# Performance work log

Hardware: AMD Instinct MI355X
Metric: run time of the kernel (lower is better)

## Reference

```python
import jax, jax.numpy as jnp
import numpy as np

HALF = 32           # (input_channels - 1) // 2
HIDDEN = 160
OUT = 32
GRU_IN = 32         # use_intensity=False -> (input_channels - 1) // 2
B, T, C = 1024, 512, 65


def setup_inputs() -> dict:
    key = jax.random.key(0)
    ks = jax.random.split(key, 10)
    times = jnp.sort(jax.random.uniform(ks[0], (T,), dtype=jnp.float32)) * 10.0
    X = jax.random.uniform(ks[1], (B, T, C), dtype=jnp.float32)
    final_index = jax.random.randint(ks[2], (B,), 0, T)
    s_ih = 1.0 / np.sqrt(HIDDEN)
    w_ih = jax.random.uniform(ks[3], (3 * HIDDEN, GRU_IN), jnp.float32, -s_ih, s_ih)
    w_hh = jax.random.uniform(ks[4], (3 * HIDDEN, HIDDEN), jnp.float32, -s_ih, s_ih)
    b_ih = jax.random.uniform(ks[5], (3 * HIDDEN,), jnp.float32, -s_ih, s_ih)
    b_hh = jax.random.uniform(ks[6], (3 * HIDDEN,), jnp.float32, -s_ih, s_ih)
    s_l = 1.0 / np.sqrt(HIDDEN)
    lin_w = jax.random.uniform(ks[7], (OUT, HIDDEN), jnp.float32, -s_l, s_l)
    lin_b = jax.random.uniform(ks[8], (OUT,), jnp.float32, -s_l, s_l)
    return {"times": times, "X": X, "final_index": final_index,
            "w_ih": w_ih, "w_hh": w_hh, "b_ih": b_ih, "b_hh": b_hh,
            "lin_w": lin_w, "lin_b": lin_b}


def _gru_cell(x, h, w_ih, w_hh, b_ih, b_hh):
    gi = x @ w_ih.T + b_ih                     # [B, 3H]
    gh = h @ w_hh.T + b_hh                     # [B, 3H]
    ir, iz, inn = jnp.split(gi, 3, axis=-1)
    hr, hz, hn = jnp.split(gh, 3, axis=-1)
    r = jax.nn.sigmoid(ir + hr)
    z = jax.nn.sigmoid(iz + hz)
    n = jnp.tanh(inn + r * hn)
    return (1.0 - z) * n + z * h


def _step(Xi, h, dt, w_ih, w_hh, b_ih, b_hh):
    # Xi: [B, C] differenced increments; channel 0 = dt increment,
    # channels 1:1+HALF = observation flags, 1+HALF: = values.
    observation = jnp.max(Xi[:, 1:1 + HALF], axis=1) > 0.5      # [B]
    Xi_piece = Xi[:, 1 + HALF:]                                  # use_intensity=False
    Xi_piece = Xi_piece.at[:, 0].add(dt)
    new_h = _gru_cell(Xi_piece, h, w_ih, w_hh, b_ih, b_hh)
    h_upd = jnp.where(observation[:, None], new_h, h)
    dt_upd = dt + jnp.where(observation, 0.0, Xi[:, 0])
    # torch skips the whole update when no sample observed this step
    any_obs = jnp.any(observation)
    h = jnp.where(any_obs, h_upd, h)
    dt = jnp.where(any_obs, dt_upd, dt)
    return h, dt


def reference(times, X, final_index, w_ih, w_hh, b_ih, b_hh, lin_w, lin_b):
    # Differencing, as in the torch forward
    Xd = X.at[:, 1:, 1:1 + HALF].add(-X[:, :-1, 1:1 + HALF])
    Xd = Xd.at[:, 0, 0].add(-times[0])
    Xd = Xd.at[:, 1:, 0].add(-times[:-1])

    z0 = jnp.zeros((B, HIDDEN), dtype=X.dtype)
    dt0 = jnp.zeros((B,), dtype=X.dtype)
    h0, dt0 = _step(Xd[:, 0], z0, dt0, w_ih, w_hh, b_ih, b_hh)

    def body(carry, Xi):
        h, dt = carry
        # evolve(h, time_diff) is identity (GRU_dt variant)
        h, dt = _step(Xi, h, dt, w_ih, w_hh, b_ih, b_hh)
        return (h, dt), h

    xs = jnp.moveaxis(Xd[:, 1:], 1, 0)                # [T-1, B, C]
    (_, _), hs = jax.lax.scan(body, (h0, dt0), xs)    # hs: [T-1, B, H]
    out = jnp.concatenate([h0[None], hs], axis=0)     # [T, B, H]
    out = jnp.moveaxis(out, 0, 1)                     # [B, T, H]
    final = jnp.take_along_axis(out, final_index[:, None, None], axis=1)[:, 0]
    return final @ lin_w.T + lin_b
```

## Files before the change

### kernel.cpp

```cpp
#include <hip/hip_runtime.h>
#include <math.h>

#define B_SZ 1024
#define T_SZ 512
#define C_CH 65
#define HID  160
#define OUTD 32
#define M_ELEM 4
#define NBLK 256
#define NTHR 640

#define LOG2E 1.4426950408889634f

#define OBS_OFF 0
#define ANY_OFF  524288
#define XD0_OFF  526336
#define S_OFF    2623488
#define WHH_OFF  6817792
#define WIH_OFF  6971392
#define XPK_OFF  7002112

typedef float f32x4_t __attribute__((ext_vector_type(4)));
typedef short bf16x8_t __attribute__((ext_vector_type(8)));
typedef unsigned u32x2_t __attribute__((ext_vector_type(2)));
typedef unsigned u32x4_t __attribute__((ext_vector_type(4)));
union frag_u { u32x4_t u; bf16x8_t h; };

__device__ __forceinline__ unsigned short f2bf(float x) {
  unsigned int u = __float_as_uint(x);
  unsigned int r = ((u >> 16) & 1u) + 0x7FFFu;
  return (unsigned short)((u + r) >> 16);
}
__device__ __forceinline__ unsigned cvt_pk_bf16(float lo, float hi) {
  unsigned r;
  asm("v_cvt_pk_bf16_f32 %0, %1, %2" : "=v"(r) : "v"(lo), "v"(hi));
  return r;
}
__device__ __forceinline__ float exp2_f(float x) {
  float r; asm("v_exp_f32 %0, %1" : "=v"(r) : "v"(x)); return r;
}
__device__ __forceinline__ float rcp_f(float x) {
  float r; asm("v_rcp_f32 %0, %1" : "=v"(r) : "v"(x)); return r;
}
__device__ __forceinline__ int tabf(int r) {
  return ((r & 1) << 1) | (((r >> 1) & 1) << 4);
}

__global__ void k_zero(unsigned* __restrict__ anyv) {
  int i = blockIdx.x * blockDim.x + threadIdx.x;
  if (i < T_SZ) anyv[i] = 0u;
}

__global__ __launch_bounds__(256) void k_prep(const float* __restrict__ X,
                                              const float* __restrict__ times,
                                              unsigned char* __restrict__ obs,
                                              unsigned* __restrict__ anyv,
                                              float* __restrict__ xd0,
                                              unsigned short* __restrict__ xpk) {
  const int b = blockIdx.x;
  const float* Xb = X + (size_t)b * T_SZ * C_CH;
  for (int t = threadIdx.x; t < T_SZ; t += 256) {
    const float* cur = Xb + t * C_CH;
    const float* prv = cur - C_CH;
    float m = -1e30f;
    if (t == 0) {
      #pragma unroll
      for (int c = 1; c <= 32; ++c) m = fmaxf(m, cur[c]);
    } else {
      #pragma unroll
      for (int c = 1; c <= 32; ++c) m = fmaxf(m, cur[c] - prv[c]);
    }
    unsigned char o = (m > 0.5f) ? (unsigned char)1 : (unsigned char)0;
    obs[(size_t)b * T_SZ + t] = o;
    if (o) atomicOr(&anyv[t], 1u);
    xd0[(size_t)b * T_SZ + t] = cur[0] - times[(t == 0) ? 0 : (t - 1)];
    unsigned short* dst = xpk + ((size_t)b * T_SZ + t) * 32;
    #pragma unroll
    for (int c = 0; c < 32; ++c) dst[c] = f2bf(cur[33 + c]);
  }
}

__global__ __launch_bounds__(64) void k_dt(const unsigned char* __restrict__ obs,
                                           const unsigned* __restrict__ anyv,
                                           const float* __restrict__ xd0,
                                           const int* __restrict__ fidx,
                                           float2* __restrict__ S) {
  const int b = blockIdx.x;
  const int lane = threadIdx.x;
  const int t0 = lane * 8;
  const unsigned long long o8 =
      *(const unsigned long long*)(obs + (size_t)b * T_SZ + t0);
  const float4* xd4 = (const float4*)(xd0 + (size_t)b * T_SZ + t0);
  const float4 xa = xd4[0], xb = xd4[1];
  const uint4* av4 = (const uint4*)(anyv + t0);
  const uint4 aa = av4[0], ab = av4[1];
  const int fi = fidx[b];
  const float xv[8] = {xa.x, xa.y, xa.z, xa.w, xb.x, xb.y, xb.z, xb.w};
  const unsigned av[8] = {aa.x, aa.y, aa.z, aa.w, ab.x, ab.y, ab.z, ab.w};
  float run = 0.f;
  float dtl[8], fl[8];
  #pragma unroll
  for (int j = 0; j < 8; ++j) {
    const int o = (int)((o8 >> (8 * j)) & 0xffULL);
    const int any = (int)av[j];
    dtl[j] = run;
    if (any && !o) run += xv[j];
    fl[j] = (any && o && (t0 + j) <= fi) ? 1.f : 0.f;
  }
  float inc = run;
  #pragma unroll
  for (int off = 1; off < 64; off <<= 1) {
    float u = __shfl_up(inc, off, 64);
    if (lane >= off) inc += u;
  }
  const float excl = inc - run;
  #pragma unroll
  for (int j = 0; j < 8; ++j)
    S[(size_t)(t0 + j) * B_SZ + b] = make_float2(excl + dtl[j], fl[j]);
}

__global__ __launch_bounds__(256) void k_pack(const float* __restrict__ w_ih,
                                              const float* __restrict__ w_hh,
                                              unsigned short* __restrict__ whh_f,
                                              unsigned short* __restrict__ wih_f) {
  int i = blockIdx.x * 256 + threadIdx.x;
  if (i < 9600) {
    int l = i & 63; int kt = (i >> 6) % 5; int g = (i / 320) % 3; int q = i / 960;
    const float scl = (g < 2) ? -LOG2E : -2.f * LOG2E;
    int row = g * 160 + q * 16 + (l & 15);
    const float* src = w_hh + (size_t)row * HID + kt * 32 + (l >> 4) * 8;
    unsigned short* dst = whh_f + (size_t)i * 8;
    #pragma unroll
    for (int j = 0; j < 8; ++j) dst[j] = f2bf(scl * src[j]);
  } else if (i < 11520) {
    int i2 = i - 9600;
    int l = i2 & 63; int g = (i2 >> 6) % 3; int q = i2 / 192;
    const float scl = (g < 2) ? -LOG2E : -2.f * LOG2E;
    int row = g * 160 + q * 16 + (l & 15);
    const float* src = w_ih + (size_t)row * 32 + (l >> 4) * 8;
    unsigned short* dst = wih_f + (size_t)i2 * 8;
    #pragma unroll
    for (int j = 0; j < 8; ++j) dst[j] = f2bf(scl * src[j]);
  }
}

#define MFMA16 __builtin_amdgcn_mfma_f32_16x16x32_bf16

__global__ __launch_bounds__(NTHR) void k_scan(
    const unsigned short* __restrict__ xpk, const int* __restrict__ fidx,
    const float* __restrict__ w_ih,
    const float* __restrict__ b_ih, const float* __restrict__ b_hh,
    const float* __restrict__ lin_w, const float* __restrict__ lin_b,
    const float2* __restrict__ Sf,
    const unsigned short* __restrict__ whh_f, const unsigned short* __restrict__ wih_f,
    float* __restrict__ out)
{
  const int b0 = blockIdx.x * M_ELEM;
  const int tid = threadIdx.x;
  const int wid = tid >> 6;
  const int lane = tid & 63;
  const int q = wid;

  __shared__ __align__(16) unsigned short hbuf[2][800];
  __shared__ __align__(16) float hm[M_ELEM][HID];

  { unsigned* hz = (unsigned*)hbuf;
    for (int i = tid; i < 800; i += NTHR) hz[i] = 0u; }

  int maxfi = 0;
  #pragma unroll
  for (int e = 0; e < M_ELEM; ++e) maxfi = max(maxfi, fidx[b0 + e]);

  const int r16 = lane & 15;
  const int g4 = lane >> 4;
  const int elA = ((r16 >> 2) + (r16 & 3)) & 3;
  const int me = g4;

  const int rb_u16 = (elA * 96 + tabf(elA)) * 2 + g4 * 8;
  const int col = q * 16 + r16;
  const int wA_u16 = (g4 * 96 + tabf(g4)) * 2 + col;

  bf16x8_t whh_v[3][5];
  bf16x8_t wih_v[3];
  #pragma unroll
  for (int g = 0; g < 3; ++g) {
    #pragma unroll
    for (int kt = 0; kt < 5; ++kt)
      whh_v[g][kt] = *(const bf16x8_t*)(whh_f + ((size_t)((q * 3 + g) * 5 + kt) * 64 + lane) * 8);
    wih_v[g] = *(const bf16x8_t*)(wih_f + ((size_t)(q * 3 + g) * 64 + lane) * 8);
  }
  const float b_r  = -LOG2E * (b_ih[col] + b_hh[col]);
  const float b_z  = -LOG2E * (b_ih[160 + col] + b_hh[160 + col]);
  const float b_ni = -2.f * LOG2E * b_ih[320 + col];
  const float b_nh = -2.f * LOG2E * b_hh[320 + col];
  const float w0r = -LOG2E * w_ih[(size_t)col * 32];
  const float w0z = -LOG2E * w_ih[(size_t)(160 + col) * 32];
  const float w0n = -2.f * LOG2E * w_ih[(size_t)(320 + col) * 32];

  float h = 0.f;
  const f32x4_t z4 = {0.f, 0.f, 0.f, 0.f};

  const unsigned short* xpk_base =
      xpk + ((size_t)(b0 + elA) * T_SZ) * 32 + g4 * 8;

  bf16x8_t xe = *(const bf16x8_t*)(xpk_base);
  bf16x8_t xo = *(const bf16x8_t*)(xpk_base + (size_t)min(1, maxfi) * 32);
  float2 se = Sf[b0 + me];
  float2 so = Sf[(size_t)min(1, maxfi) * B_SZ + b0 + me];
  __syncthreads();

  const int NSTEP = (maxfi + 2) & ~1;

#define BODY(T, PB, XI, SI)                                                \
  {                                                                        \
                         \
    frag_u hf0, hf1, hf2, hf3, hf4;                                        \
    {                                                                      \
      const u32x2_t* hp = (const u32x2_t*)&hbuf[PB][rb_u16];               \
      u32x2_t l0 = hp[0],  u0 = hp[1];                                     \
      u32x2_t l1 = hp[8],  u1 = hp[9];                                     \
      u32x2_t l2 = hp[16], u2 = hp[17];                                    \
      u32x2_t l3 = hp[24], u3 = hp[25];                                    \
      u32x2_t l4 = hp[32], u4 = hp[33];                                    \
      hf0.u = (u32x4_t){l0.x, l0.y, u0.x, u0.y};                           \
      hf1.u = (u32x4_t){l1.x, l1.y, u1.x, u1.y};                           \
      hf2.u = (u32x4_t){l2.x, l2.y, u2.x, u2.y};                           \
      hf3.u = (u32x4_t){l3.x, l3.y, u3.x, u3.y};                           \
      hf4.u = (u32x4_t){l4.x, l4.y, u4.x, u4.y};                           \
    }                                                                      \
          \
    f32x4_t ginr = MFMA16(XI, wih_v[0], z4, 0, 0, 0);                      \
    f32x4_t ginz = MFMA16(XI, wih_v[1], z4, 0, 0, 0);                      \
    f32x4_t ginn = MFMA16(XI, wih_v[2], z4, 0, 0, 0);                      \
               \
    const float crI = fmaf(SI.x, w0r, b_r);                                \
    const float czI = fmaf(SI.x, w0z, b_z);                                \
    const float cnI = fmaf(SI.x, w0n, b_ni);                               \
    const float flI = SI.y;                                                \
                    \
    __builtin_amdgcn_s_setprio(1);                                         \
    f32x4_t ra  = MFMA16(hf0.h, whh_v[0][0], ginr, 0, 0, 0);               \
    f32x4_t za  = MFMA16(hf0.h, whh_v[1][0], ginz, 0, 0, 0);               \
    f32x4_t nha = MFMA16(hf0.h, whh_v[2][0], z4,   0, 0, 0);               \
    f32x4_t rb  = MFMA16(hf2.h, whh_v[0][2], z4,   0, 0, 0);               \
    f32x4_t zb  = MFMA16(hf2.h, whh_v[1][2], z4,   0, 0, 0);               \
    f32x4_t nhb = MFMA16(hf3.h, whh_v[2][3], z4,   0, 0, 0);               \
    ra  = MFMA16(hf1.h, whh_v[0][1], ra,  0, 0, 0);                        \
    za  = MFMA16(hf1.h, whh_v[1][1], za,  0, 0, 0);                        \
    nha = MFMA16(hf1.h, whh_v[2][1], nha, 0, 0, 0);                        \
    rb  = MFMA16(hf3.h, whh_v[0][3], rb,  0, 0, 0);                        \
    zb  = MFMA16(hf3.h, whh_v[1][3], zb,  0, 0, 0);                        \
    nhb = MFMA16(hf4.h, whh_v[2][4], nhb, 0, 0, 0);                        \
    nha = MFMA16(hf2.h, whh_v[2][2], nha, 0, 0, 0);                        \
    rb  = MFMA16(hf4.h, whh_v[0][4], rb,  0, 0, 0);                        \
    zb  = MFMA16(hf4.h, whh_v[1][4], zb,  0, 0, 0);                        \
    __builtin_amdgcn_s_setprio(0);                                         \
              \
    {                                                                      \
      const int tl = min((T) + 2, T_SZ - 1);                               \
      XI = *(const bf16x8_t*)(xpk_base + (size_t)tl * 32);                 \
      SI = Sf[(size_t)tl * B_SZ + b0 + me];                                \
    }                                                                      \
                         \
    {                                                                      \
      const float pre_r = (ra[0] + rb[0]) + crI;                           \
      const float rr = rcp_f(1.f + exp2_f(pre_r));                         \
      const float pre_z = (za[0] + zb[0]) + czI;                           \
      const float zz = rcp_f(1.f + exp2_f(pre_z));                         \
      float u = (ginn[0] + cnI) + rr * ((nha[0] + nhb[0]) + b_nh);         \
      u = fminf(u, 60.f);                                                  \
      const float e = exp2_f(u);                                           \
      const float nn = (1.f - e) * rcp_f(1.f + e);                         \
      const float upd = nn + zz * (h - nn);                                \
      h = h + flI * (upd - h);                                             \
    }                                                                      \
                                             \
    hbuf[PB ^ 1][wA_u16] = (unsigned short)cvt_pk_bf16(h, h);              \
    __syncthreads();                                                       \
  }

  for (int t = 0; t < NSTEP; t += 2) {
    BODY(t,     0, xe, se);
    BODY(t + 1, 1, xo, so);
  }
#undef BODY

  hm[me][col] = h;
  __syncthreads();
  if (tid < M_ELEM * OUTD) {
    const int e = tid >> 5, o = tid & 31;
    const float4* lw = (const float4*)(lin_w + o * HID);
    const float4* hv = (const float4*)(&hm[e][0]);
    float a0 = 0.f, a1 = 0.f, a2 = 0.f, a3 = 0.f;
    #pragma unroll
    for (int k = 0; k < HID / 4; ++k) {
      float4 w = lw[k], hh = hv[k];
      a0 = fmaf(w.x, hh.x, a0); a1 = fmaf(w.y, hh.y, a1);
      a2 = fmaf(w.z, hh.z, a2); a3 = fmaf(w.w, hh.w, a3);
    }
    out[(size_t)(b0 + e) * OUTD + o] = lin_b[o] + (a0 + a1) + (a2 + a3);
  }
}

extern "C" void kernel_launch(void* const* d_in, const int* in_sizes, int n_in,
                              void* d_out, int out_size, void* d_ws, size_t ws_size,
                              hipStream_t stream) {
  const float* times = (const float*)d_in[0];
  const float* X     = (const float*)d_in[1];
  const int*   fidx  = (const int*)d_in[2];
  const float* w_ih  = (const float*)d_in[3];
  const float* w_hh  = (const float*)d_in[4];
  const float* b_ih  = (const float*)d_in[5];
  const float* b_hh  = (const float*)d_in[6];
  const float* lin_w = (const float*)d_in[7];
  const float* lin_b = (const float*)d_in[8];
  float* outp = (float*)d_out;

  unsigned char* obsb = (unsigned char*)d_ws + OBS_OFF;
  unsigned* anyv = (unsigned*)((char*)d_ws + ANY_OFF);
  float* xd0 = (float*)((char*)d_ws + XD0_OFF);
  float2* S = (float2*)((char*)d_ws + S_OFF);
  unsigned short* whh_f = (unsigned short*)((char*)d_ws + WHH_OFF);
  unsigned short* wih_f = (unsigned short*)((char*)d_ws + WIH_OFF);
  unsigned short* xpk = (unsigned short*)((char*)d_ws + XPK_OFF);

  k_zero<<<1, 512, 0, stream>>>(anyv);
  k_prep<<<B_SZ, 256, 0, stream>>>(X, times, obsb, anyv, xd0, xpk);
  k_dt<<<B_SZ, 64, 0, stream>>>(obsb, anyv, xd0, fidx, S);
  k_pack<<<45, 256, 0, stream>>>(w_ih, w_hh, whh_f, wih_f);
  k_scan<<<NBLK, NTHR, 0, stream>>>(xpk, fidx, w_ih, b_ih, b_hh,
                                    lin_w, lin_b, S, whh_f, wih_f, outp);
}
```

Measured before the change: 367.2 us.

## Stage per-step scalars in LDS and use single 16-byte hidden-state fragment loads

The per-step scalar array S is now stored batch-major and preloaded into shared memory for the block's four elements, so each step reads it from LDS instead of issuing a dependent global load. The hidden-state buffer padding (tabf) changes so each MFMA fragment can be read with one 16-byte LDS load instead of two 8-byte loads plus repacking. The gate update math is rewritten as fused multiply-adds, with tanh computed as 2*sigmoid-1. In exchange the block uses about 16KB more LDS, and the initial staging adds a short prologue.

```diff
diff --git a/kernel.cpp b/kernel.cpp
--- a/kernel.cpp
+++ b/kernel.cpp
@@ -22,9 +22,6 @@
 
 typedef float f32x4_t __attribute__((ext_vector_type(4)));
 typedef short bf16x8_t __attribute__((ext_vector_type(8)));
-typedef unsigned u32x2_t __attribute__((ext_vector_type(2)));
-typedef unsigned u32x4_t __attribute__((ext_vector_type(4)));
-union frag_u { u32x4_t u; bf16x8_t h; };
 
 __device__ __forceinline__ unsigned short f2bf(float x) {
   unsigned int u = __float_as_uint(x);
@@ -43,7 +40,7 @@
   float r; asm("v_rcp_f32 %0, %1" : "=v"(r) : "v"(x)); return r;
 }
 __device__ __forceinline__ int tabf(int r) {
-  return ((r & 1) << 1) | (((r >> 1) & 1) << 4);
+  return ((r & 1) << 2) | (((r >> 1) & 1) << 4);
 }
 
 __global__ void k_zero(unsigned* __restrict__ anyv) {
@@ -116,7 +113,7 @@
   const float excl = inc - run;
   #pragma unroll
   for (int j = 0; j < 8; ++j)
-    S[(size_t)(t0 + j) * B_SZ + b] = make_float2(excl + dtl[j], fl[j]);
+    S[(size_t)b * T_SZ + t0 + j] = make_float2(excl + dtl[j], fl[j]);
 }
 
 __global__ __launch_bounds__(256) void k_pack(const float* __restrict__ w_ih,
@@ -162,10 +159,15 @@
   const int q = wid;
 
   __shared__ __align__(16) unsigned short hbuf[2][800];
+  __shared__ __align__(8) float2 s_lds[T_SZ * M_ELEM];
   __shared__ __align__(16) float hm[M_ELEM][HID];
 
   { unsigned* hz = (unsigned*)hbuf;
     for (int i = tid; i < 800; i += NTHR) hz[i] = 0u; }
+  for (int i = tid; i < T_SZ * M_ELEM; i += NTHR) {
+    const int e = i >> 9, t = i & (T_SZ - 1);
+    s_lds[t * M_ELEM + e] = Sf[(size_t)(b0 + e) * T_SZ + t];
+  }
 
   int maxfi = 0;
   #pragma unroll
@@ -174,7 +176,6 @@
   const int r16 = lane & 15;
   const int g4 = lane >> 4;
   const int elA = ((r16 >> 2) + (r16 & 3)) & 3;
-  const int me = g4;
 
   const int rb_u16 = (elA * 96 + tabf(elA)) * 2 + g4 * 8;
   const int col = q * 16 + r16;
@@ -205,74 +206,59 @@
 
   bf16x8_t xe = *(const bf16x8_t*)(xpk_base);
   bf16x8_t xo = *(const bf16x8_t*)(xpk_base + (size_t)min(1, maxfi) * 32);
-  float2 se = Sf[b0 + me];
-  float2 so = Sf[(size_t)min(1, maxfi) * B_SZ + b0 + me];
   __syncthreads();
 
   const int NSTEP = (maxfi + 2) & ~1;
 
-#define BODY(T, PB, XI, SI)                                                \
+#define BODY(T, PB, XI)                                                    \
   {                                                                        \
-                         \
-    frag_u hf0, hf1, hf2, hf3, hf4;                                        \
-    {                                                                      \
-      const u32x2_t* hp = (const u32x2_t*)&hbuf[PB][rb_u16];               \
-      u32x2_t l0 = hp[0],  u0 = hp[1];                                     \
-      u32x2_t l1 = hp[8],  u1 = hp[9];                                     \
-      u32x2_t l2 = hp[16], u2 = hp[17];                                    \
-      u32x2_t l3 = hp[24], u3 = hp[25];                                    \
-      u32x2_t l4 = hp[32], u4 = hp[33];                                    \
-      hf0.u = (u32x4_t){l0.x, l0.y, u0.x, u0.y};                           \
-      hf1.u = (u32x4_t){l1.x, l1.y, u1.x, u1.y};                           \
-      hf2.u = (u32x4_t){l2.x, l2.y, u2.x, u2.y};                           \
-      hf3.u = (u32x4_t){l3.x, l3.y, u3.x, u3.y};                           \
-      hf4.u = (u32x4_t){l4.x, l4.y, u4.x, u4.y};                           \
-    }                                                                      \
+                \
+    bf16x8_t hf0 = *(const bf16x8_t*)&hbuf[PB][rb_u16];                    \
+    bf16x8_t hf1 = *(const bf16x8_t*)&hbuf[PB][rb_u16 + 32];               \
+    bf16x8_t hf2 = *(const bf16x8_t*)&hbuf[PB][rb_u16 + 64];               \
+    bf16x8_t hf3 = *(const bf16x8_t*)&hbuf[PB][rb_u16 + 96];               \
+    bf16x8_t hf4 = *(const bf16x8_t*)&hbuf[PB][rb_u16 + 128];              \
           \
     f32x4_t ginr = MFMA16(XI, wih_v[0], z4, 0, 0, 0);                      \
     f32x4_t ginz = MFMA16(XI, wih_v[1], z4, 0, 0, 0);                      \
     f32x4_t ginn = MFMA16(XI, wih_v[2], z4, 0, 0, 0);                      \
-               \
-    const float crI = fmaf(SI.x, w0r, b_r);                                \
-    const float czI = fmaf(SI.x, w0z, b_z);                                \
-    const float cnI = fmaf(SI.x, w0n, b_ni);                               \
-    const float flI = SI.y;                                                \
+            \
+    const float2 sI = s_lds[(T) * M_ELEM + g4];                            \
+    const float crI = fmaf(sI.x, w0r, b_r);                                \
+    const float czI = fmaf(sI.x, w0z, b_z);                                \
+    const float cnI = fmaf(sI.x, w0n, b_ni);                               \
                     \
     __builtin_amdgcn_s_setprio(1);                                         \
-    f32x4_t ra  = MFMA16(hf0.h, whh_v[0][0], ginr, 0, 0, 0);               \
-    f32x4_t za  = MFMA16(hf0.h, whh_v[1][0], ginz, 0, 0, 0);               \
-    f32x4_t nha = MFMA16(hf0.h, whh_v[2][0], z4,   0, 0, 0);               \
-    f32x4_t rb  = MFMA16(hf2.h, whh_v[0][2], z4,   0, 0, 0);               \
-    f32x4_t zb  = MFMA16(hf2.h, whh_v[1][2], z4,   0, 0, 0);               \
-    f32x4_t nhb = MFMA16(hf3.h, whh_v[2][3], z4,   0, 0, 0);               \
-    ra  = MFMA16(hf1.h, whh_v[0][1], ra,  0, 0, 0);                        \
-    za  = MFMA16(hf1.h, whh_v[1][1], za,  0, 0, 0);                        \
-    nha = MFMA16(hf1.h, whh_v[2][1], nha, 0, 0, 0);                        \
-    rb  = MFMA16(hf3.h, whh_v[0][3], rb,  0, 0, 0);                        \
-    zb  = MFMA16(hf3.h, whh_v[1][3], zb,  0, 0, 0);                        \
-    nhb = MFMA16(hf4.h, whh_v[2][4], nhb, 0, 0, 0);                        \
-    nha = MFMA16(hf2.h, whh_v[2][2], nha, 0, 0, 0);                        \
-    rb  = MFMA16(hf4.h, whh_v[0][4], rb,  0, 0, 0);                        \
-    zb  = MFMA16(hf4.h, whh_v[1][4], zb,  0, 0, 0);                        \
+    f32x4_t ra  = MFMA16(hf0, whh_v[0][0], ginr, 0, 0, 0);                 \
+    f32x4_t za  = MFMA16(hf0, whh_v[1][0], ginz, 0, 0, 0);                 \
+    f32x4_t nha = MFMA16(hf0, whh_v[2][0], z4,   0, 0, 0);                 \
+    f32x4_t rb  = MFMA16(hf2, whh_v[0][2], z4,   0, 0, 0);                 \
+    f32x4_t zb  = MFMA16(hf2, whh_v[1][2], z4,   0, 0, 0);                 \
+    f32x4_t nhb = MFMA16(hf3, whh_v[2][3], z4,   0, 0, 0);                 \
+    ra  = MFMA16(hf1, whh_v[0][1], ra,  0, 0, 0);                          \
+    za  = MFMA16(hf1, whh_v[1][1], za,  0, 0, 0);                          \
+    nha = MFMA16(hf1, whh_v[2][1], nha, 0, 0, 0);                          \
+    rb  = MFMA16(hf3, whh_v[0][3], rb,  0, 0, 0);                          \
+    zb  = MFMA16(hf3, whh_v[1][3], zb,  0, 0, 0);                          \
+    nhb = MFMA16(hf4, whh_v[2][4], nhb, 0, 0, 0);                          \
+    nha = MFMA16(hf2, whh_v[2][2], nha, 0, 0, 0);                          \
+    rb  = MFMA16(hf4, whh_v[0][4], rb,  0, 0, 0);                          \
+    zb  = MFMA16(hf4, whh_v[1][4], zb,  0, 0, 0);                          \
     __builtin_amdgcn_s_setprio(0);                                         \
               \
     {                                                                      \
       const int tl = min((T) + 2, T_SZ - 1);                               \
       XI = *(const bf16x8_t*)(xpk_base + (size_t)tl * 32);                 \
-      SI = Sf[(size_t)tl * B_SZ + b0 + me];                                \
     }                                                                      \
                          \
     {                                                                      \
-      const float pre_r = (ra[0] + rb[0]) + crI;                           \
-      const float rr = rcp_f(1.f + exp2_f(pre_r));                         \
-      const float pre_z = (za[0] + zb[0]) + czI;                           \
-      const float zz = rcp_f(1.f + exp2_f(pre_z));                         \
+      const float rr = rcp_f(1.f + exp2_f((ra[0] + rb[0]) + crI));         \
+      const float zz = rcp_f(1.f + exp2_f((za[0] + zb[0]) + czI));         \
       float u = (ginn[0] + cnI) + rr * ((nha[0] + nhb[0]) + b_nh);         \
       u = fminf(u, 60.f);                                                  \
-      const float e = exp2_f(u);                                           \
-      const float nn = (1.f - e) * rcp_f(1.f + e);                         \
-      const float upd = nn + zz * (h - nn);                                \
-      h = h + flI * (upd - h);                                             \
+      const float nn = fmaf(2.f, rcp_f(1.f + exp2_f(u)), -1.f);            \
+      const float w = fmaf(-sI.y, zz, sI.y);                \
+      h = fmaf(w, nn - h, h);                                              \
     }                                                                      \
                                              \
     hbuf[PB ^ 1][wA_u16] = (unsigned short)cvt_pk_bf16(h, h);              \
@@ -280,12 +266,12 @@
   }
 
   for (int t = 0; t < NSTEP; t += 2) {
-    BODY(t,     0, xe, se);
-    BODY(t + 1, 1, xo, so);
+    BODY(t,     0, xe);
+    BODY(t + 1, 1, xo);
   }
 #undef BODY
 
-  hm[me][col] = h;
+  hm[g4][col] = h;
   __syncthreads();
   if (tid < M_ELEM * OUTD) {
     const int e = tid >> 5, o = tid & 31;
```

Measured after the change: 393.0 us. 7.0% more time.
